# Optimization experiments

Measured on AMD Instinct MI355X. Metric: run time of the kernel, lower is better.

The kernel has to match this reference:

```python
import jax, jax.numpy as jnp
import numpy as np

NEARZERO = 1e-5
NMUL = 16
LENF = 15
PARAM_BOUNDS = [
    ("parBETA", 1.0, 6.0), ("parFC", 50.0, 1000.0), ("parK0", 0.05, 0.9),
    ("parK1", 0.01, 0.5), ("parK2", 0.001, 0.2), ("parLP", 0.2, 1.0),
    ("parPERC", 0.0, 10.0), ("parUZL", 0.0, 100.0), ("parTT", -2.5, 2.5),
    ("parCFMAX", 0.5, 10.0), ("parCFR", 0.0, 0.1), ("parCWH", 0.0, 0.2),
    ("parBETAET", 0.3, 5.0), ("parC", 0.0, 1.0),
]
ROUT_A = (0.0, 2.9)
ROUT_B = (0.0, 6.5)


def setup_inputs() -> dict:
    key = jax.random.key(0)
    k1, k2, k3, k4 = jax.random.split(key, 4)
    Nstep, Ngrid = 365, 2000
    return {
        "x_hydro_model": jax.random.uniform(k1, (Nstep, Ngrid, 3), jnp.float32),
        "c_hydro_model": jax.random.normal(k2, (Ngrid, 1), jnp.float32),
        "params_raw": jax.random.uniform(k3, (Nstep, Ngrid, len(PARAM_BOUNDS), NMUL), jnp.float32),
        "conv_params_hydro": jax.random.uniform(k4, (Ngrid, 2), jnp.float32),
    }


def _uh_gamma(a, b, lenF=LENF):
    # a, b: [Ngrid]; returns normalized gamma unit hydrograph [lenF, Ngrid]
    aa = jax.nn.relu(a)[None, :] + 0.1
    theta = jax.nn.relu(b)[None, :] + 0.5
    t = jnp.arange(0.5, float(lenF), dtype=jnp.float32)[:, None]
    denom = jnp.exp(jax.lax.lgamma(aa)) * theta ** aa
    w = (t ** (aa - 1.0)) * jnp.exp(-t / theta) / denom
    return w / w.sum(0)


def _hbv(x_hydro_model, params_raw, conv_params_hydro):
    Nstep, Ngrid, _ = x_hydro_model.shape
    # static parameters: last timestep, scaled to physical bounds -> [Ngrid, NMUL]
    p = {name: params_raw[-1, :, i, :] * (hi - lo) + lo
         for i, (name, lo, hi) in enumerate(PARAM_BOUNDS)}
    # forcings broadcast over the nmul component axis
    Pm = jnp.broadcast_to(x_hydro_model[:, :, 0:1], (Nstep, Ngrid, NMUL))
    Tm = jnp.broadcast_to(x_hydro_model[:, :, 1:2], (Nstep, Ngrid, NMUL))
    PETm = jnp.broadcast_to(x_hydro_model[:, :, 2:3], (Nstep, Ngrid, NMUL))

    s0 = jnp.full((Ngrid, NMUL), 0.001, jnp.float32)
    init = (s0, s0, s0, s0, s0)  # SNOWPACK, MELTWATER, SM, SUZ, SLZ

    def step(state, inp):
        SNOWPACK, MELTWATER, SM, SUZ, SLZ = state
        P, T, PET = inp
        RAIN = jnp.where(T >= p["parTT"], P, 0.0)
        SNOW = jnp.where(T < p["parTT"], P, 0.0)
        SNOWPACK = SNOWPACK + SNOW
        melt = jnp.clip(p["parCFMAX"] * (T - p["parTT"]), 0.0, None)
        melt = jnp.minimum(melt, SNOWPACK)
        MELTWATER = MELTWATER + melt
        SNOWPACK = jnp.maximum(SNOWPACK - melt, NEARZERO)
        refreezing = jnp.clip(p["parCFR"] * p["parCFMAX"] * (p["parTT"] - T), 0.0, None)
        refreezing = jnp.minimum(refreezing, MELTWATER)
        SNOWPACK = SNOWPACK + refreezing
        MELTWATER = jnp.maximum(MELTWATER - refreezing, NEARZERO)
        tosoil = jnp.clip(MELTWATER - p["parCWH"] * SNOWPACK, 0.0, None)
        MELTWATER = jnp.maximum(MELTWATER - tosoil, NEARZERO)
        soil_wetness = jnp.clip((SM / p["parFC"]) ** p["parBETA"], 0.0, 1.0)
        recharge = (RAIN + tosoil) * soil_wetness
        SM = SM + RAIN + tosoil - recharge
        excess = jnp.clip(SM - p["parFC"], 0.0, None)
        SM = jnp.maximum(SM - excess, NEARZERO)
        evapfactor = jnp.clip((SM / (p["parLP"] * p["parFC"])) ** p["parBETAET"], 0.0, 1.0)
        ETact = jnp.minimum(SM, PET * evapfactor)
        SM = jnp.maximum(SM - ETact, NEARZERO)
        capillary = jnp.minimum(SLZ, p["parC"] * SLZ * (1.0 - jnp.clip(SM / p["parFC"], None, 1.0)))
        SM = jnp.maximum(SM + capillary, NEARZERO)
        SLZ = jnp.maximum(SLZ - capillary, NEARZERO)
        SUZ = SUZ + recharge + excess
        PERC = jnp.minimum(SUZ, p["parPERC"])
        SUZ = SUZ - PERC
        Q0 = p["parK0"] * jnp.clip(SUZ - p["parUZL"], 0.0, None)
        SUZ = SUZ - Q0
        Q1 = p["parK1"] * SUZ
        SUZ = SUZ - Q1
        SLZ = SLZ + PERC
        Q2 = p["parK2"] * SLZ
        SLZ = SLZ - Q2
        return (SNOWPACK, MELTWATER, SM, SUZ, SLZ), Q0 + Q1 + Q2

    _, Qsimmu = jax.lax.scan(step, init, (Pm, Tm, PETm))  # [Nstep, Ngrid, NMUL]
    Qsimavg = Qsimmu.mean(-1)                             # [Nstep, Ngrid] (muwts=None)

    # gamma unit-hydrograph routing = per-basin causal grouped conv1d
    tempa = conv_params_hydro[:, 0] * (ROUT_A[1] - ROUT_A[0]) + ROUT_A[0]
    tempb = conv_params_hydro[:, 1] * (ROUT_B[1] - ROUT_B[0]) + ROUT_B[0]
    UH = _uh_gamma(tempa, tempb, LENF)                    # [LENF, Ngrid]
    conv1 = jax.vmap(lambda xg, wg: jnp.convolve(xg, wg)[:Nstep])
    Qsrout = conv1(Qsimavg.T, UH.T).T                     # [Nstep, Ngrid]
    return Qsrout[:, :, None]                             # flow_sim [Nstep, Ngrid, 1]


def reference(x_hydro_model, c_hydro_model, params_raw, conv_params_hydro):
    return _hbv(x_hydro_model, params_raw, conv_params_hydro)
```

## Files before the change

kernel.cpp:

```cpp
#include <hip/hip_runtime.h>


#define LENF 15

__device__ __forceinline__ float flog2(float x) { return __builtin_amdgcn_logf(x); }
__device__ __forceinline__ float fexp2(float x) { return __builtin_amdgcn_exp2f(x); }
__device__ __forceinline__ float fpow(float x, float y) { return fexp2(y * flog2(x)); }

template <int CTRL>
__device__ __forceinline__ float dpp_add(float x) {
    int p = __builtin_amdgcn_update_dpp(0, __float_as_int(x), CTRL, 0xF, 0xF, true);
    return x + __int_as_float(p);
}

__global__ __launch_bounds__(64) void hbv_kernel(
    const float* __restrict__ x,
    const float* __restrict__ praw,
    const float* __restrict__ convp,
    float* __restrict__ out,
    int Nstep, int Ngrid)
{
    const int tid = threadIdx.x;
    const int gl  = tid >> 4;
    const int m   = tid & 15;
    const int g0  = blockIdx.x * 4;
    const int g   = g0 + gl;

    __shared__ float4 lds4[1104];
    float* ldsx = (float*)lds4;
    {
        const float4* src = (const float4*)(x + (size_t)g0 * 3);
        const int row4   = (Ngrid * 3) >> 2;
        const int total4 = Nstep * 3;
        float4 tmp[18];
        #pragma unroll
        for (int k = 0; k < 18; ++k) {
            int j = tid + (k << 6);
            if (j < total4) {
                int t = j / 3, q = j - t * 3;
                tmp[k] = src[(size_t)t * row4 + q];
            }
        }
        #pragma unroll
        for (int k = 0; k < 18; ++k) {
            int j = tid + (k << 6);
            if (j < total4) lds4[j] = tmp[k];
        }
    }
    __syncthreads();

    const float lo[14] = {1.0f, 50.0f, 0.05f, 0.01f, 0.001f, 0.2f, 0.0f, 0.0f,
                          -2.5f, 0.5f, 0.0f, 0.0f, 0.3f, 0.0f};
    const float hi[14] = {6.0f, 1000.0f, 0.9f, 0.5f, 0.2f, 1.0f, 10.0f, 100.0f,
                          2.5f, 10.0f, 0.1f, 0.2f, 5.0f, 1.0f};
    float par[14];
    {
        const float* pr = praw + ((size_t)(Nstep - 1) * Ngrid + g) * 14 * 16 + m;
        #pragma unroll
        for (int i = 0; i < 14; ++i)
            par[i] = fmaf(pr[i * 16], hi[i] - lo[i], lo[i]);
    }
    const float pBETA = par[0], pFC = par[1], pK0 = par[2], pK1 = par[3], pK2 = par[4],
                pLP = par[5], pPERC = par[6], pUZL = par[7], pTT = par[8], pCFMAX = par[9],
                pCFR = par[10], pCWH = par[11], pBETAET = par[12], pC = par[13];
    const float invFC    = 1.0f / pFC;
    const float invLPFC  = 1.0f / (pLP * pFC);
    const float cfrcfmax = pCFR * pCFMAX;

    float uh[LENF];
    {
        float a  = convp[g * 2 + 0] * 2.9f;
        float bb = convp[g * 2 + 1] * 6.5f;
        float aa = fmaxf(a, 0.0f) + 0.1f;
        float th = fmaxf(bb, 0.0f) + 0.5f;
        float am1 = aa - 1.0f;
        float c1  = 1.4426950408889634f / th;
        const float L[LENF] = {
            -1.0f, 0.5849625007f, 1.3219280949f, 1.8073549221f, 2.1699250014f,
            2.4594316186f, 2.7004397181f, 2.9068905956f, 3.0874628413f, 3.2479275134f,
            3.3923174228f, 3.5235619561f, 3.6438561898f, 3.7548875022f, 3.8579809951f};
        float s = 0.0f;
        #pragma unroll
        for (int k = 0; k < LENF; ++k) {
            float t = (float)k + 0.5f;
            float w = fexp2(fmaf(am1, L[k], -t * c1));
            uh[k] = w;
            s += w;
        }
        float is = 1.0f / s;
        #pragma unroll
        for (int k = 0; k < LENF; ++k) uh[k] *= is;
    }

    const float NZ = 1e-5f;
    float SNOWPACK = 1e-3f, MELTWATER = 1e-3f, SM = 1e-3f, SUZ = 1e-3f, SLZ = 1e-3f;
    float h[LENF];
    #pragma unroll
    for (int k = 0; k < LENF; ++k) h[k] = 0.0f;

    int b = gl * 3;
    float Pc = ldsx[b], Tc = ldsx[b + 1], Ec = ldsx[b + 2];
    float* orow = out + g;

    for (int t = 0; t < Nstep; ++t) {
        b += 12;
        float Pn = ldsx[b], Tn = ldsx[b + 1], En = ldsx[b + 2];

        float P = Pc, T = Tc, PET = Ec;
        bool warm  = (T >= pTT);
        float RAIN = warm ? P : 0.0f;
        float SNOW = warm ? 0.0f : P;
        SNOWPACK += SNOW;
        float melt = fminf(fmaxf(pCFMAX * (T - pTT), 0.0f), SNOWPACK);
        MELTWATER += melt;
        SNOWPACK = fmaxf(SNOWPACK - melt, NZ);
        float refr = fminf(fmaxf(cfrcfmax * (pTT - T), 0.0f), MELTWATER);
        SNOWPACK += refr;
        MELTWATER = fmaxf(MELTWATER - refr, NZ);
        float tosoil = fmaxf(fmaf(-pCWH, SNOWPACK, MELTWATER), 0.0f);
        MELTWATER = fmaxf(MELTWATER - tosoil, NZ);
        float sw = fminf(fpow(SM * invFC, pBETA), 1.0f);
        float rt = RAIN + tosoil;
        float recharge = rt * sw;
        SM = SM + rt - recharge;
        float excess = fmaxf(SM - pFC, 0.0f);
        SM = fmaxf(SM - excess, NZ);
        float ev = fminf(fpow(SM * invLPFC, pBETAET), 1.0f);
        float ETact = fminf(SM, PET * ev);
        SM = fmaxf(SM - ETact, NZ);
        float cap = fminf(SLZ, pC * SLZ * (1.0f - fminf(SM * invFC, 1.0f)));
        SM  = fmaxf(SM + cap, NZ);
        SLZ = fmaxf(SLZ - cap, NZ);
        SUZ = SUZ + recharge + excess;
        float perc = fminf(SUZ, pPERC);
        SUZ -= perc;
        float Q0 = pK0 * fmaxf(SUZ - pUZL, 0.0f);
        SUZ -= Q0;
        float Q1 = pK1 * SUZ;
        SUZ -= Q1;
        SLZ += perc;
        float Q2 = pK2 * SLZ;
        SLZ -= Q2;
        float q = Q0 + Q1 + Q2;

        float qs = q;
        qs = dpp_add<0x121>(qs);
        qs = dpp_add<0x122>(qs);
        qs = dpp_add<0x124>(qs);
        qs = dpp_add<0x128>(qs);
        float qavg = qs * 0.0625f;

        #pragma unroll
        for (int k = LENF - 1; k > 0; --k) h[k] = h[k - 1];
        h[0] = qavg;
        float r0 = 0.0f, r1 = 0.0f, r2 = 0.0f;
        #pragma unroll
        for (int k = 0; k + 2 < LENF; k += 3) {
            r0 = fmaf(uh[k], h[k], r0);
            r1 = fmaf(uh[k + 1], h[k + 1], r1);
            r2 = fmaf(uh[k + 2], h[k + 2], r2);
        }
        if (m == 0) orow[(size_t)t * Ngrid] = r0 + r1 + r2;

        Pc = Pn; Tc = Tn; Ec = En;
    }
}

extern "C" void kernel_launch(void* const* d_in, const int* in_sizes, int n_in,
                              void* d_out, int out_size, void* d_ws, size_t ws_size,
                              hipStream_t stream) {
    const float* x     = (const float*)d_in[0];
    const float* praw  = (const float*)d_in[2];
    const float* convp = (const float*)d_in[3];
    float* out = (float*)d_out;

    int Ngrid = in_sizes[3] / 2;
    int Nstep = in_sizes[0] / (3 * Ngrid);
    int blocks = Ngrid / 4;

    hbv_kernel<<<blocks, 64, 0, stream>>>(x, praw, convp, out, Nstep, Ngrid);
}
```

Baseline: 795.7 us.

## Move unit-hydrograph convolution out of serial recurrence into parallel post-pass

Each step's averaged runoff is now written to a shared-memory buffer instead of being convolved inside the time loop. After a barrier, the 16 lanes of each basin each convolve a contiguous chunk of timesteps with the 15-tap hydrograph. This removes the register shifts and FMAs from the latency-bound sequential loop, where all 16 lanes used to repeat them, and it coalesces the output stores into a separate phase. The cost is extra shared memory, a barrier, and a short tail pass. The launch bounds also now state one block per multiprocessor.

```diff
diff --git a/kernel.cpp b/kernel.cpp
--- a/kernel.cpp
+++ b/kernel.cpp
@@ -13,7 +13,7 @@
     return x + __int_as_float(p);
 }
 
-__global__ __launch_bounds__(64) void hbv_kernel(
+__global__ __launch_bounds__(64, 1) void hbv_kernel(
     const float* __restrict__ x,
     const float* __restrict__ praw,
     const float* __restrict__ convp,
@@ -27,7 +27,9 @@
     const int g   = g0 + gl;
 
     __shared__ float4 lds4[1104];
+    __shared__ float  qbuf[366 * 4];
     float* ldsx = (float*)lds4;
+
     {
         const float4* src = (const float4*)(x + (size_t)g0 * 3);
         const int row4   = (Ngrid * 3) >> 2;
@@ -94,13 +96,10 @@
 
     const float NZ = 1e-5f;
     float SNOWPACK = 1e-3f, MELTWATER = 1e-3f, SM = 1e-3f, SUZ = 1e-3f, SLZ = 1e-3f;
-    float h[LENF];
-    #pragma unroll
-    for (int k = 0; k < LENF; ++k) h[k] = 0.0f;
 
     int b = gl * 3;
     float Pc = ldsx[b], Tc = ldsx[b + 1], Ec = ldsx[b + 2];
-    float* orow = out + g;
+    float* qrow = qbuf + gl;
 
     for (int t = 0; t < Nstep; ++t) {
         b += 12;
@@ -148,21 +147,29 @@
         qs = dpp_add<0x122>(qs);
         qs = dpp_add<0x124>(qs);
         qs = dpp_add<0x128>(qs);
-        float qavg = qs * 0.0625f;
-
-        #pragma unroll
-        for (int k = LENF - 1; k > 0; --k) h[k] = h[k - 1];
-        h[0] = qavg;
-        float r0 = 0.0f, r1 = 0.0f, r2 = 0.0f;
-        #pragma unroll
-        for (int k = 0; k + 2 < LENF; k += 3) {
-            r0 = fmaf(uh[k], h[k], r0);
-            r1 = fmaf(uh[k + 1], h[k + 1], r1);
-            r2 = fmaf(uh[k + 2], h[k + 2], r2);
-        }
-        if (m == 0) orow[(size_t)t * Ngrid] = r0 + r1 + r2;
+        if (m == 0) qrow[t * 4] = qs * 0.0625f;
 
         Pc = Pn; Tc = Tn; Ec = En;
+    }
+    __syncthreads();
+
+    const int chunk = (Nstep + 15) >> 4;
+    int t0 = m * chunk;
+    int t1 = min(t0 + chunk, Nstep);
+    float w[LENF];
+    #pragma unroll
+    for (int k = 0; k < LENF; ++k) {
+        int tt = t0 - k;
+        w[k] = (tt >= 0) ? qrow[tt * 4] : 0.0f;
+    }
+    for (int t = t0; t < t1; ++t) {
+        float acc = 0.0f;
+        #pragma unroll
+        for (int k = 0; k < LENF; ++k) acc = fmaf(uh[k], w[k], acc);
+        out[(size_t)t * Ngrid + g] = acc;
+        #pragma unroll
+        for (int k = LENF - 1; k > 0; --k) w[k] = w[k - 1];
+        w[0] = (t + 1 < Nstep) ? qrow[(t + 1) * 4] : 0.0f;
     }
 }
 
```

Measured after the change: 779.8 us. -2.0%, faster.
